# Performance work log

Hardware: AMD Instinct MI355X
Metric: run time of the kernel (lower is better)

Reference implementation:

```python
import jax, jax.numpy as jnp
import numpy as np
import math

# dims
B, T, HFEAT, E = 32, 8, 128, 128
NUM_CLS, NUM_GLOBAL = 4, 2
NSP = NUM_CLS + NUM_GLOBAL            # 6 special tokens
SCALES = (1, 4, 8)
WINDOW = 4
NHEAD = 8
DH = E // NHEAD                        # 16
NLAYERS = 2                            # blocks per scale = ceil(6/3)
NS = len(SCALES)
F = 512                                # dim_feedforward
ROPE_BASE = 100000.0
NEG = -1e9


def setup_inputs() -> dict:
    key = jax.random.key(0)
    ks = jax.random.split(key, 16)
    def rn(k, shape, s=0.02):
        return jax.random.normal(k, shape, jnp.float32) * s
    inp = {
        'embeddings': jax.random.normal(ks[0], (B, T, NSP + HFEAT, E), jnp.float32),
        'cls_tokens': rn(ks[1], (NUM_CLS, E)),
        'global_tokens': rn(ks[2], (NUM_GLOBAL, E)),
        'Wq': rn(ks[3], (NS, NLAYERS, E, E)),
        'bq': jnp.zeros((NS, NLAYERS, E), jnp.float32),
        'Wk': rn(ks[4], (NS, NLAYERS, E, E)),
        'bk': jnp.zeros((NS, NLAYERS, E), jnp.float32),
        'Wv': rn(ks[5], (NS, NLAYERS, E, E)),
        'bv': jnp.zeros((NS, NLAYERS, E), jnp.float32),
        'Wo': rn(ks[6], (NS, NLAYERS, E, E)),
        'bo': jnp.zeros((NS, NLAYERS, E), jnp.float32),
        'ln1_g': jnp.ones((NS, NLAYERS, E), jnp.float32),
        'ln1_b': jnp.zeros((NS, NLAYERS, E), jnp.float32),
        'ln2_g': jnp.ones((NS, NLAYERS, E), jnp.float32),
        'ln2_b': jnp.zeros((NS, NLAYERS, E), jnp.float32),
        'W1': rn(ks[7], (NS, NLAYERS, E, F)),
        'b1': jnp.zeros((NS, NLAYERS, F), jnp.float32),
        'W2': rn(ks[8], (NS, NLAYERS, F, E)),
        'b2': jnp.zeros((NS, NLAYERS, E), jnp.float32),
        'out_g': jnp.ones((E,), jnp.float32),
        'out_b': jnp.zeros((E,), jnp.float32),
    }
    return inp


def _layernorm(x, g, b, eps=1e-5):
    mu = x.mean(-1, keepdims=True)
    var = ((x - mu) ** 2).mean(-1, keepdims=True)
    return (x - mu) * jax.lax.rsqrt(var + eps) * g + b


def _rope(x):
    # x: (BT, L, H, DH); rotate-half RoPE over head dim
    L = x.shape[1]
    half = DH // 2
    inv = ROPE_BASE ** (-jnp.arange(half, dtype=jnp.float32) / half)
    ang = jnp.arange(L, dtype=jnp.float32)[:, None] * inv[None, :]   # (L, half)
    cos = jnp.cos(ang)[None, :, None, :]
    sin = jnp.sin(ang)[None, :, None, :]
    x1, x2 = x[..., :half], x[..., half:]
    return jnp.concatenate([x1 * cos - x2 * sin, x1 * sin + x2 * cos], axis=-1)


def _sparse_bias(L):
    # global(first NSP) rows/cols fully connected, others window +-WINDOW, diag allowed
    i = jnp.arange(L)
    allowed = (jnp.abs(i[:, None] - i[None, :]) <= WINDOW) | (i[:, None] < NSP) | (i[None, :] < NSP)
    return jnp.where(allowed, 0.0, NEG).astype(jnp.float32)  # (L, L) additive


def _encoder(x, s, Wq, bq, Wk, bk, Wv, bv, Wo, bo, ln1_g, ln1_b, ln2_g, ln2_b, W1, b1, W2, b2, bias):
    # x: (BT, L, E); pre-norm transformer encoder with RoPE attention
    BT, L, _ = x.shape
    for l in range(NLAYERS):
        h = _layernorm(x, ln1_g[s, l], ln1_b[s, l])
        q = (h @ Wq[s, l] + bq[s, l]).reshape(BT, L, NHEAD, DH)
        k = (h @ Wk[s, l] + bk[s, l]).reshape(BT, L, NHEAD, DH)
        v = (h @ Wv[s, l] + bv[s, l]).reshape(BT, L, NHEAD, DH)
        q, k = _rope(q), _rope(k)
        scores = jnp.einsum('blhd,bmhd->bhlm', q, k) / math.sqrt(DH) + bias[None, None]
        attn = jax.nn.softmax(scores, axis=-1)
        o = jnp.einsum('bhlm,bmhd->blhd', attn, v).reshape(BT, L, E)
        x = x + o @ Wo[s, l] + bo[s, l]
        h2 = _layernorm(x, ln2_g[s, l], ln2_b[s, l])
        x = x + jax.nn.gelu(h2 @ W1[s, l] + b1[s, l]) @ W2[s, l] + b2[s, l]
    return x


def reference(embeddings, cls_tokens, global_tokens, Wq, bq, Wk, bk, Wv, bv, Wo, bo,
              ln1_g, ln1_b, ln2_g, ln2_b, W1, b1, W2, b2, out_g, out_b):
    Bb, Tt, HC, Ee = embeddings.shape
    feats = embeddings[..., NSP:, :]                                 # (B,T,H,E)
    specials = jnp.broadcast_to(
        jnp.concatenate([cls_tokens, global_tokens], axis=0)[None, None],
        (Bb, Tt, NSP, Ee))
    cls_per_scale = []
    for s, g in enumerate(SCALES):
        H = feats.shape[2]
        K = H // g  # H divisible by all scales
        grouped = feats.reshape(Bb, Tt, K, g, Ee).mean(axis=3)       # contiguous mean grouping
        seq = jnp.concatenate([specials, grouped], axis=2)           # (B,T,L,E)
        L = NSP + K
        x = seq.reshape(Bb * Tt, L, Ee)
        bias = _sparse_bias(L)
        out = _encoder(x, s, Wq, bq, Wk, bk, Wv, bv, Wo, bo,
                       ln1_g, ln1_b, ln2_g, ln2_b, W1, b1, W2, b2, bias)
        cls_per_scale.append(out.reshape(Bb, Tt, L, Ee)[..., :NUM_CLS, :])
    cls_out = jnp.stack(cls_per_scale, axis=0).mean(axis=0)          # (B,T,num_cls,E)
    cls_out = _layernorm(cls_out, out_g, out_b)
    return cls_out.reshape(Bb, Tt, NUM_CLS * Ee)
```

## Files before the change

### kernel.cpp

```cpp
#include <hip/hip_runtime.h>
#include <hip/hip_bf16.h>

#define BT     256
#define EDIM   128
#define NSP    6
#define RT     49664
#define O1     34304
#define O2     44032
#define KSTR   20

typedef unsigned short u16;
typedef short s16x8 __attribute__((ext_vector_type(8)));
typedef float f32x4 __attribute__((ext_vector_type(4)));

__device__ __forceinline__ float u2f(u16 u){ union{unsigned i; float f;} v; v.i=((unsigned)u)<<16; return v.f; }
__device__ __forceinline__ u16 f2u(float f){
  union{float f; unsigned i;} v; v.f = f;
  unsigned r = v.i + 0x7FFF + ((v.i >> 16) & 1);
  return (u16)(r >> 16);
}
__device__ __forceinline__ float ldin(const void* p, size_t idx, int flag){
  return flag ? u2f(((const u16*)p)[idx]) : ((const float*)p)[idx];
}
__device__ __forceinline__ void unp8(uint4 v, float* f){
  f[0]=u2f((u16)(v.x)); f[1]=u2f((u16)(v.x>>16));
  f[2]=u2f((u16)(v.y)); f[3]=u2f((u16)(v.y>>16));
  f[4]=u2f((u16)(v.z)); f[5]=u2f((u16)(v.z>>16));
  f[6]=u2f((u16)(v.w)); f[7]=u2f((u16)(v.w>>16));
}

__device__ __forceinline__ void rowinfo(int row, int& s, int& r, int& L, int& g){
  if (row < O1){ s=0; r=row;    L=134; g=1; }
  else if (row < O2){ s=1; r=row-O1; L=38; g=4; }
  else { s=2; r=row-O2; L=22; g=8; }
}

__device__ __forceinline__ float ropeInv(int d){
  const float t[8] = {1.f, 0.23713737f, 0.056234132f, 0.013335214f,
                      3.1622777e-3f, 7.4989421e-4f, 1.7782794e-4f, 4.2169650e-5f};
  return t[d];
}

__device__ __forceinline__ float gelu_f(float x){
  float u = x*(1.5957691216f + 0.0713548162f*x*x);
  return x * __builtin_amdgcn_rcpf(1.f + __expf(-u));
}

__global__ void detect_k(const void* ln1g, int* flagp){
  unsigned v = *(const unsigned*)ln1g;
  *flagp = (v == 0x3F803F80u) ? 1 : 0;
}

struct CArg { const void* src; unsigned dstoff; unsigned n; unsigned inblk; unsigned outblk; };
struct CArgs { CArg a[12]; };
__global__ __launch_bounds__(256) void conv_k(CArgs ca, u16* stage, const int* flagp){
  int i = blockIdx.y;
  int flag = *flagp;
  const CArg& c = ca.a[i];
  for (unsigned idx = blockIdx.x*256u + threadIdx.x; idx < c.n; idx += gridDim.x*256u){
    unsigned blk = idx / c.inblk, r = idx % c.inblk;
    float v = flag ? u2f(((const u16*)c.src)[idx]) : ((const float*)c.src)[idx];
    stage[c.dstoff + blk*c.outblk + r] = flag ? ((const u16*)c.src)[idx] : f2u(v);
  }
}

__global__ __launch_bounds__(256) void convw_k(const void* s0, const void* s1, const void* s2,
                                               u16* dst, int K, int N, int Nsrc, const int* flagp)
{
  int flag = *flagp;
  const void* srcs[3] = {s0, s1, s2};
  int total = 6 * K * N;
  for (int idx = blockIdx.x*256 + threadIdx.x; idx < total; idx += gridDim.x*256) {
    int blk = idx / (K*N);
    int rem = idx % (K*N);
    int j = rem & 7;
    int t = rem >> 3;
    int n = t % N;
    int ck = t / N;
    int k = ck*8 + j;
    int w = n / Nsrc;
    int nn = n - w*Nsrc;
    size_t sidx = (size_t)blk*K*Nsrc + (size_t)k*Nsrc + nn;
    dst[idx] = flag ? ((const u16*)srcs[w])[sidx] : f2u(((const float*)srcs[w])[sidx]);
  }
}

__global__ __launch_bounds__(256) void build_k(const void* __restrict__ emb,
                                               const void* __restrict__ cls,
                                               const void* __restrict__ glob,
                                               float* __restrict__ x,
                                               u16* __restrict__ H,
                                               const u16* __restrict__ lnG,
                                               const u16* __restrict__ lnB,
                                               const int* flagp)
{
  int flag = *flagp;
  int row = blockIdx.x*4 + (threadIdx.x >> 6);
  int lane = threadIdx.x & 63;
  int s, r, L, g; rowinfo(row, s, r, L, g);
  int seq = r / L, pos = r % L;
  float v0, v1;
  if (pos < NSP) {
    const void* src = (pos < 4) ? cls : glob;
    int p = (pos < 4) ? pos : pos - 4;
    v0 = ldin(src, p*EDIM + lane, flag);
    v1 = ldin(src, p*EDIM + 64 + lane, flag);
  } else {
    int k = pos - NSP;
    size_t base = ((size_t)seq*134 + NSP + (size_t)k*g)*EDIM + lane;
    float s0 = 0.f, s1 = 0.f;
    for (int j = 0; j < g; j++) {
      s0 += ldin(emb, base + (size_t)j*EDIM, flag);
      s1 += ldin(emb, base + (size_t)j*EDIM + 64, flag);
    }
    float inv = 1.f/(float)g;
    v0 = s0*inv; v1 = s1*inv;
  }
  x[(size_t)row*EDIM + lane]      = v0;
  x[(size_t)row*EDIM + 64 + lane] = v1;
  float sum = v0 + v1, ss = v0*v0 + v1*v1;
  #pragma unroll
  for (int off = 32; off; off >>= 1) { sum += __shfl_xor(sum, off); ss += __shfl_xor(ss, off); }
  float mu = sum * (1.f/128.f);
  float var = ss * (1.f/128.f) - mu*mu;
  float rs = rsqrtf(var + 1e-5f);
  const u16* gp = lnG + s*2*EDIM;
  const u16* bp = lnB + s*2*EDIM;
  H[(size_t)row*EDIM + lane]      = f2u((v0-mu)*rs*u2f(gp[lane])    + u2f(bp[lane]));
  H[(size_t)row*EDIM + 64 + lane] = f2u((v1-mu)*rs*u2f(gp[64+lane]) + u2f(bp[64+lane]));
}

__global__ __launch_bounds__(256) void qkv_k(
    const u16* __restrict__ A,
    const u16* __restrict__ Wt, const u16* __restrict__ Bias,
    u16* __restrict__ C, int layer)
{
  const int row0 = blockIdx.x * 64;
  const int n0 = blockIdx.y * 128;
  const int s = row0 < O1 ? 0 : (row0 < O2 ? 1 : 2);
  const int sl = s*2 + layer;
  const u16* Wp = Wt + (size_t)sl*49152;
  const u16* bp = Bias + (size_t)sl*384 + n0;
  const int tid = threadIdx.x;
  const int lane = tid & 63, w = tid >> 6;
  const int g = lane >> 4, l15 = lane & 15;

  s16x8 af[4];
  {
    const u16* arow = A + (size_t)(row0 + w*16 + l15)*128;
    #pragma unroll
    for (int ks = 0; ks < 4; ks++) af[ks] = *(const s16x8*)(arow + (ks*4 + g)*8);
  }
  const u16* wbase = Wp + ((size_t)g*384 + n0 + l15)*8;

  f32x4 acc[8];
  #pragma unroll
  for (int nt = 0; nt < 8; nt++) acc[nt] = (f32x4){0.f,0.f,0.f,0.f};
  #pragma unroll
  for (int ks = 0; ks < 4; ks++) {
    s16x8 bw[8];
    #pragma unroll
    for (int nt = 0; nt < 8; nt++)
      bw[nt] = *(const s16x8*)(wbase + (size_t)ks*12288 + nt*128);
    #pragma unroll
    for (int nt = 0; nt < 8; nt++)
      acc[nt] = __builtin_amdgcn_mfma_f32_16x16x32_bf16(af[ks], bw[nt], acc[nt], 0, 0, 0);
  }

  float bb[8];
  #pragma unroll
  for (int nt = 0; nt < 8; nt++) bb[nt] = u2f(bp[nt*16 + l15]);
  #pragma unroll
  for (int reg = 0; reg < 4; reg++) {
    int row = row0 + w*16 + g*4 + reg;
    #pragma unroll
    for (int nt = 0; nt < 8; nt++)
      C[(size_t)row*384 + n0 + nt*16 + l15] = f2u(acc[nt][reg] + bb[nt]);
  }
}

template<int LNFUSE>
__global__ __launch_bounds__(256) __attribute__((amdgpu_waves_per_eu(2,3))) void woffn_k(
    const u16* __restrict__ A,
    const u16* __restrict__ Wot, const u16* __restrict__ Bo,
    const u16* __restrict__ W1t, const u16* __restrict__ B1,
    const u16* __restrict__ W2t, const u16* __restrict__ B2,
    float* __restrict__ X,
    u16* __restrict__ H,
    const u16* __restrict__ ln2G, const u16* __restrict__ ln2B,
    const u16* __restrict__ ln1G, const u16* __restrict__ ln1B,
    int layer)
{
  __shared__ u16 Hs[4][16*136];
  __shared__ u16 Ts[2][4][16*40];
  const int row0 = blockIdx.x * 64;
  const int s = row0 < O1 ? 0 : (row0 < O2 ? 1 : 2);
  const int sl = s*2 + layer;
  const u16* Wop = Wot + (size_t)sl*16384;
  const u16* bop = Bo  + sl*128;
  const u16* W1p = W1t + (size_t)sl*65536;
  const u16* b1p = B1  + sl*512;
  const u16* W2p = W2t + (size_t)sl*65536;
  const u16* b2p = B2  + sl*128;
  const int tid = threadIdx.x;
  const int lane = tid & 63, w = tid >> 6;
  const int g = lane >> 4, l15 = lane & 15;

  s16x8 af[4];
  {
    const u16* arow = A + (size_t)(row0 + w*16 + l15)*128;
    #pragma unroll
    for (int ks = 0; ks < 4; ks++) af[ks] = *(const s16x8*)(arow + (ks*4 + g)*8);
  }
  const u16* wobase = Wop + ((size_t)g*128 + l15)*8;

  f32x4 acc2[8];
  #pragma unroll
  for (int nt = 0; nt < 8; nt++) acc2[nt] = (f32x4){0.f,0.f,0.f,0.f};
  #pragma unroll
  for (int ks = 0; ks < 4; ks++) {
    s16x8 bw[8];
    #pragma unroll
    for (int nt = 0; nt < 8; nt++)
      bw[nt] = *(const s16x8*)(wobase + ((size_t)ks*4096 + nt*128));
    #pragma unroll
    for (int nt = 0; nt < 8; nt++)
      acc2[nt] = __builtin_amdgcn_mfma_f32_16x16x32_bf16(af[ks], bw[nt], acc2[nt], 0, 0, 0);
  }

  {
    float gam[8], bet[8], bo_[8];
    const u16* gp  = ln2G + sl*EDIM;
    const u16* bp2 = ln2B + sl*EDIM;
    #pragma unroll
    for (int nt = 0; nt < 8; nt++) {
      gam[nt] = u2f(gp[nt*16+l15]); bet[nt] = u2f(bp2[nt*16+l15]);
      bo_[nt] = u2f(bop[nt*16+l15]);
    }
    #pragma unroll
    for (int reg = 0; reg < 4; reg++) {
      int row = row0 + w*16 + g*4 + reg;
      float vals[8], ps = 0.f, pss = 0.f;
      #pragma unroll
      for (int nt = 0; nt < 8; nt++) {
        float v = acc2[nt][reg] + bo_[nt] + X[(size_t)row*128 + nt*16 + l15];
        vals[nt] = v; ps += v; pss += v*v;
      }
      #pragma unroll
      for (int off = 1; off < 16; off <<= 1) { ps += __shfl_xor(ps, off); pss += __shfl_xor(pss, off); }
      float mu = ps * (1.f/128.f);
      float var = pss * (1.f/128.f) - mu*mu;
      float rs = rsqrtf(var + 1e-5f);
      #pragma unroll
      for (int nt = 0; nt < 8; nt++) {
        acc2[nt][reg] = vals[nt];
        Hs[w][(g*4+reg)*136 + nt*16 + l15] = f2u((vals[nt]-mu)*rs*gam[nt] + bet[nt]);
      }
    }
  }

  s16x8 hf[4];
  #pragma unroll
  for (int ks = 0; ks < 4; ks++) hf[ks] = *(const s16x8*)&Hs[w][l15*136 + (ks*4+g)*8];

  const u16* w1base = W1p + ((size_t)g*512 + l15)*8;
  const u16* w2base = W2p + ((size_t)g*128 + l15)*8;

  s16x8 bw1[8];
  #pragma unroll
  for (int ks = 0; ks < 4; ks++)
    #pragma unroll
    for (int nt = 0; nt < 2; nt++)
      bw1[ks*2+nt] = *(const s16x8*)(w1base + (size_t)(ks*2048 + nt*16)*8);

  {
    f32x4 acc1[2];
    acc1[0] = (f32x4){0.f,0.f,0.f,0.f};
    acc1[1] = (f32x4){0.f,0.f,0.f,0.f};
    #pragma unroll
    for (int ks = 0; ks < 4; ks++) {
      acc1[0] = __builtin_amdgcn_mfma_f32_16x16x32_bf16(hf[ks], bw1[ks*2+0], acc1[0], 0, 0, 0);
      acc1[1] = __builtin_amdgcn_mfma_f32_16x16x32_bf16(hf[ks], bw1[ks*2+1], acc1[1], 0, 0, 0);
    }
    #pragma unroll
    for (int ks = 0; ks < 4; ks++)
      #pragma unroll
      for (int nt = 0; nt < 2; nt++)
        bw1[ks*2+nt] = *(const s16x8*)(w1base + (size_t)(ks*2048 + 32 + nt*16)*8);
    #pragma unroll
    for (int nt = 0; nt < 2; nt++) {
      float bb1 = u2f(b1p[nt*16 + l15]);
      #pragma unroll
      for (int reg = 0; reg < 4; reg++)
        Ts[0][w][(g*4+reg)*40 + nt*16 + l15] = f2u(gelu_f(acc1[nt][reg] + bb1));
    }
  }

  #pragma unroll
  for (int i = 1; i < 16; i++) {
    const int f0 = i*32, fp = f0 - 32;
    u16* tsC = &Ts[i & 1][w][0];
    const u16* tsP = &Ts[(i & 1) ^ 1][w][0];

    s16x8 bw2a[4];
    #pragma unroll
    for (int nt = 0; nt < 4; nt++)
      bw2a[nt] = *(const s16x8*)(w2base + (size_t)(fp*16 + nt*16)*8);
    s16x8 af2p = *(const s16x8*)(tsP + l15*40 + g*8);

    f32x4 acc1[2];
    acc1[0] = (f32x4){0.f,0.f,0.f,0.f};
    acc1[1] = (f32x4){0.f,0.f,0.f,0.f};
    #pragma unroll
    for (int ks = 0; ks < 4; ks++) {
      acc1[0] = __builtin_amdgcn_mfma_f32_16x16x32_bf16(hf[ks], bw1[ks*2+0], acc1[0], 0, 0, 0);
      acc1[1] = __builtin_amdgcn_mfma_f32_16x16x32_bf16(hf[ks], bw1[ks*2+1], acc1[1], 0, 0, 0);
    }
    {
      const int fn = (f0 + 32) & 511;
      #pragma unroll
      for (int ks = 0; ks < 4; ks++)
        #pragma unroll
        for (int nt = 0; nt < 2; nt++)
          bw1[ks*2+nt] = *(const s16x8*)(w1base + (size_t)(ks*2048 + fn + nt*16)*8);
    }
    s16x8 bw2b[4];
    #pragma unroll
    for (int nt = 0; nt < 4; nt++)
      bw2b[nt] = *(const s16x8*)(w2base + (size_t)(fp*16 + 64 + nt*16)*8);

    #pragma unroll
    for (int nt = 0; nt < 2; nt++) {
      float bb1 = u2f(b1p[f0 + nt*16 + l15]);
      #pragma unroll
      for (int reg = 0; reg < 4; reg++)
        tsC[(g*4+reg)*40 + nt*16 + l15] = f2u(gelu_f(acc1[nt][reg] + bb1));
    }

    #pragma unroll
    for (int nt = 0; nt < 4; nt++)
      acc2[nt] = __builtin_amdgcn_mfma_f32_16x16x32_bf16(af2p, bw2a[nt], acc2[nt], 0, 0, 0);
    #pragma unroll
    for (int nt = 0; nt < 4; nt++)
      acc2[4+nt] = __builtin_amdgcn_mfma_f32_16x16x32_bf16(af2p, bw2b[nt], acc2[4+nt], 0, 0, 0);
  }

  {
    s16x8 af2p = *(const s16x8*)&Ts[1][w][l15*40 + g*8];
    #pragma unroll
    for (int nt = 0; nt < 8; nt++) {
      s16x8 b = *(const s16x8*)(w2base + (size_t)(480*16 + nt*16)*8);
      acc2[nt] = __builtin_amdgcn_mfma_f32_16x16x32_bf16(af2p, b, acc2[nt], 0, 0, 0);
    }
  }

  float bb2[8];
  #pragma unroll
  for (int nt = 0; nt < 8; nt++) bb2[nt] = u2f(b2p[nt*16 + l15]);

  if (LNFUSE) {
    float gam[8], bet[8];
    const u16* gp  = ln1G + (s*2+1)*EDIM;
    const u16* bpn = ln1B + (s*2+1)*EDIM;
    #pragma unroll
    for (int nt = 0; nt < 8; nt++) { gam[nt] = u2f(gp[nt*16+l15]); bet[nt] = u2f(bpn[nt*16+l15]); }
    #pragma unroll
    for (int reg = 0; reg < 4; reg++) {
      int row = row0 + w*16 + g*4 + reg;
      float vals[8], ps = 0.f, pss = 0.f;
      #pragma unroll
      for (int nt = 0; nt < 8; nt++) {
        float v = acc2[nt][reg] + bb2[nt];
        vals[nt] = v; ps += v; pss += v*v;
      }
      #pragma unroll
      for (int off = 1; off < 16; off <<= 1) { ps += __shfl_xor(ps, off); pss += __shfl_xor(pss, off); }
      float mu = ps * (1.f/128.f);
      float var = pss * (1.f/128.f) - mu*mu;
      float rs = rsqrtf(var + 1e-5f);
      #pragma unroll
      for (int nt = 0; nt < 8; nt++) {
        size_t cidx = (size_t)row*128 + nt*16 + l15;
        X[cidx] = vals[nt];
        H[cidx] = f2u((vals[nt]-mu)*rs*gam[nt] + bet[nt]);
      }
    }
  } else {
    #pragma unroll
    for (int reg = 0; reg < 4; reg++) {
      int row = row0 + w*16 + g*4 + reg;
      #pragma unroll
      for (int nt = 0; nt < 8; nt++) {
        size_t cidx = (size_t)row*128 + nt*16 + l15;
        X[cidx] = acc2[nt][reg] + bb2[nt];
      }
    }
  }
}

__global__ __launch_bounds__(128) void attn_k(const u16* __restrict__ qkv, u16* __restrict__ o)
{
  __shared__ float Ks[134*KSTR];
  __shared__ float Vs[134*KSTR];
  int gseq = blockIdx.x, hd = blockIdx.y;
  int L, base;
  if (gseq < 256)      { L = 134; base = gseq*134; }
  else if (gseq < 512) { L = 38;  base = O1 + (gseq-256)*38; }
  else                 { L = 22;  base = O2 + (gseq-512)*22; }
  int tid = threadIdx.x;
  for (int u = tid; u < L*2; u += 128) {
    int kv = u & 1, row = u >> 1;
    const u16* p = qkv + (size_t)(base+row)*384 + 128 + kv*128 + hd*16;
    uint4 w0 = *(const uint4*)p, w1 = *(const uint4*)(p+8);
    float f[16];
    unp8(w0, f); unp8(w1, f+8);
    if (kv == 0) {
      #pragma unroll
      for (int d = 0; d < 8; d++) {
        float ang = (float)row * ropeInv(d);
        float cs = __cosf(ang), sn = __sinf(ang);
        float a = f[d], b = f[d+8];
        f[d]   = a*cs - b*sn;
        f[d+8] = a*sn + b*cs;
      }
    }
    float* dst = (kv ? Vs : Ks) + row*KSTR;
    #pragma unroll
    for (int d = 0; d < 16; d++) dst[d] = f[d];
  }
  __syncthreads();

  for (int it = tid; it < L - NSP; it += 128) {
    int row = NSP + it;
    const u16* qp = qkv + (size_t)(base+row)*384 + hd*16;
    uint4 w0 = *(const uint4*)qp, w1 = *(const uint4*)(qp+8);
    float q[16]; unp8(w0, q); unp8(w1, q+8);
    #pragma unroll
    for (int d = 0; d < 8; d++) {
      float ang = (float)row * ropeInv(d);
      float cs = __cosf(ang), sn = __sinf(ang);
      float a = q[d], b = q[d+8];
      q[d]   = a*cs - b*sn;
      q[d+8] = a*sn + b*cs;
    }
    float m = -1e30f, l = 0.f, oa[16] = {};
    auto step = [&](int j){
      const float4* kr = (const float4*)(Ks + j*KSTR);
      float4 k0 = kr[0], k1 = kr[1], k2 = kr[2], k3 = kr[3];
      float sc = q[0]*k0.x + q[1]*k0.y + q[2]*k0.z + q[3]*k0.w
               + q[4]*k1.x + q[5]*k1.y + q[6]*k1.z + q[7]*k1.w
               + q[8]*k2.x + q[9]*k2.y + q[10]*k2.z + q[11]*k2.w
               + q[12]*k3.x + q[13]*k3.y + q[14]*k3.z + q[15]*k3.w;
      sc *= 0.25f;
      float nm = fmaxf(m, sc);
      float scale = __expf(m - nm);
      float pexp = __expf(sc - nm);
      l = l*scale + pexp;
      const float4* vr = (const float4*)(Vs + j*KSTR);
      float4 v0 = vr[0], v1 = vr[1], v2 = vr[2], v3 = vr[3];
      oa[0]=oa[0]*scale+pexp*v0.x;  oa[1]=oa[1]*scale+pexp*v0.y;
      oa[2]=oa[2]*scale+pexp*v0.z;  oa[3]=oa[3]*scale+pexp*v0.w;
      oa[4]=oa[4]*scale+pexp*v1.x;  oa[5]=oa[5]*scale+pexp*v1.y;
      oa[6]=oa[6]*scale+pexp*v1.z;  oa[7]=oa[7]*scale+pexp*v1.w;
      oa[8]=oa[8]*scale+pexp*v2.x;  oa[9]=oa[9]*scale+pexp*v2.y;
      oa[10]=oa[10]*scale+pexp*v2.z; oa[11]=oa[11]*scale+pexp*v2.w;
      oa[12]=oa[12]*scale+pexp*v3.x; oa[13]=oa[13]*scale+pexp*v3.y;
      oa[14]=oa[14]*scale+pexp*v3.z; oa[15]=oa[15]*scale+pexp*v3.w;
      m = nm;
    };
    #pragma unroll
    for (int j = 0; j < NSP; j++) step(j);
    int jlo = (row-4 > NSP) ? row-4 : NSP;
    int jhi = (row+4 < L-1) ? row+4 : L-1;
    for (int j = jlo; j <= jhi; j++) step(j);
    float invl = 1.f/l;
    u16* op = o + (size_t)(base+row)*EDIM + hd*16;
    #pragma unroll
    for (int d = 0; d < 16; d++) op[d] = f2u(oa[d]*invl);
  }

  if (tid < 96) {
    int row = tid >> 4;
    int u = tid & 15;
    const u16* qp = qkv + (size_t)(base+row)*384 + hd*16;
    uint4 w0 = *(const uint4*)qp, w1 = *(const uint4*)(qp+8);
    float q[16]; unp8(w0, q); unp8(w1, q+8);
    #pragma unroll
    for (int d = 0; d < 8; d++) {
      float ang = (float)row * ropeInv(d);
      float cs = __cosf(ang), sn = __sinf(ang);
      float a = q[d], b = q[d+8];
      q[d]   = a*cs - b*sn;
      q[d+8] = a*sn + b*cs;
    }
    float m = -1e30f, l = 0.f, oa[16] = {};
    for (int j = u; j < L; j += 16) {
      const float4* kr = (const float4*)(Ks + j*KSTR);
      float4 k0 = kr[0], k1 = kr[1], k2 = kr[2], k3 = kr[3];
      float sc = q[0]*k0.x + q[1]*k0.y + q[2]*k0.z + q[3]*k0.w
               + q[4]*k1.x + q[5]*k1.y + q[6]*k1.z + q[7]*k1.w
               + q[8]*k2.x + q[9]*k2.y + q[10]*k2.z + q[11]*k2.w
               + q[12]*k3.x + q[13]*k3.y + q[14]*k3.z + q[15]*k3.w;
      sc *= 0.25f;
      float nm = fmaxf(m, sc);
      float scale = __expf(m - nm);
      float pexp = __expf(sc - nm);
      l = l*scale + pexp;
      const float4* vr = (const float4*)(Vs + j*KSTR);
      float4 v0 = vr[0], v1 = vr[1], v2 = vr[2], v3 = vr[3];
      oa[0]=oa[0]*scale+pexp*v0.x;  oa[1]=oa[1]*scale+pexp*v0.y;
      oa[2]=oa[2]*scale+pexp*v0.z;  oa[3]=oa[3]*scale+pexp*v0.w;
      oa[4]=oa[4]*scale+pexp*v1.x;  oa[5]=oa[5]*scale+pexp*v1.y;
      oa[6]=oa[6]*scale+pexp*v1.z;  oa[7]=oa[7]*scale+pexp*v1.w;
      oa[8]=oa[8]*scale+pexp*v2.x;  oa[9]=oa[9]*scale+pexp*v2.y;
      oa[10]=oa[10]*scale+pexp*v2.z; oa[11]=oa[11]*scale+pexp*v2.w;
      oa[12]=oa[12]*scale+pexp*v3.x; oa[13]=oa[13]*scale+pexp*v3.y;
      oa[14]=oa[14]*scale+pexp*v3.z; oa[15]=oa[15]*scale+pexp*v3.w;
      m = nm;
    }
    #pragma unroll
    for (int off = 1; off < 16; off <<= 1) {
      float m2 = __shfl_xor(m, off);
      float l2 = __shfl_xor(l, off);
      float nm = fmaxf(m, m2);
      float s1 = __expf(m - nm), s2 = __expf(m2 - nm);
      #pragma unroll
      for (int d = 0; d < 16; d++) {
        float o2 = __shfl_xor(oa[d], off);
        oa[d] = oa[d]*s1 + o2*s2;
      }
      l = l*s1 + l2*s2;
      m = nm;
    }
    if (u == 0) {
      float invl = 1.f/l;
      u16* op = o + (size_t)(base+row)*EDIM + hd*16;
      #pragma unroll
      for (int d = 0; d < 16; d++) op[d] = f2u(oa[d]*invl);
    }
  }
}

__global__ __launch_bounds__(256) void final_k(const float* __restrict__ x,
                                               const u16* __restrict__ G,
                                               const u16* __restrict__ Bt,
                                               void* __restrict__ out, const int* flagp)
{
  int flag = *flagp;
  int wid = threadIdx.x >> 6, lane = threadIdx.x & 63;
  int idx = blockIdx.x*4 + wid;
  int seq = idx >> 2, c = idx & 3;
  size_t r0 = ((size_t)seq*134 + c)*EDIM;
  size_t r1 = ((size_t)O1 + (size_t)seq*38 + c)*EDIM;
  size_t r2 = ((size_t)O2 + (size_t)seq*22 + c)*EDIM;
  float v0 = (x[r0+lane]    + x[r1+lane]    + x[r2+lane])    * (1.f/3.f);
  float v1 = (x[r0+64+lane] + x[r1+64+lane] + x[r2+64+lane]) * (1.f/3.f);
  float sum = v0 + v1;
  #pragma unroll
  for (int off = 32; off; off >>= 1) sum += __shfl_xor(sum, off);
  float mu = sum * (1.f/128.f);
  float d0 = v0 - mu, d1 = v1 - mu;
  float var = d0*d0 + d1*d1;
  #pragma unroll
  for (int off = 32; off; off >>= 1) var += __shfl_xor(var, off);
  var *= (1.f/128.f);
  float rs = rsqrtf(var + 1e-5f);
  float o0 = d0*rs*u2f(G[lane])    + u2f(Bt[lane]);
  float o1 = d1*rs*u2f(G[64+lane]) + u2f(Bt[64+lane]);
  size_t oi0 = (size_t)seq*512 + c*128 + lane;
  if (flag) { ((u16*)out)[oi0] = f2u(o0); ((u16*)out)[oi0+64] = f2u(o1); }
  else      { ((float*)out)[oi0] = o0;    ((float*)out)[oi0+64] = o1; }
}

#define S_WQKV 0u
#define S_BQKV 294912u
#define S_WO   297216u
#define S_BO   395520u
#define S_W1   396288u
#define S_B1   789504u
#define S_W2   792576u
#define S_B2   1185792u
#define S_L1G  1186560u
#define S_L1B  1187328u
#define S_L2G  1188096u
#define S_L2B  1188864u
#define S_OG   1189632u
#define S_OB   1189760u

extern "C" void kernel_launch(void* const* d_in, const int* in_sizes, int n_in,
                              void* d_out, int out_size, void* d_ws, size_t ws_size,
                              hipStream_t stream) {
  char* wsb = (char*)d_ws;
  int*   flagp = (int*)wsb;
  u16*   stage = (u16*)(wsb + 64);
  float* x     = (float*)(wsb + (size_t)2379840);
  u16*   h     = (u16*)(wsb + (size_t)27807808);
  u16*   qkv   = (u16*)(wsb + (size_t)40521792);

  detect_k<<<1, 1, 0, stream>>>(d_in[11], flagp);

  CArgs ca;
  CArg list[12] = {
    { d_in[4],  S_BQKV,       768, 128, 384 },
    { d_in[6],  S_BQKV+128u,  768, 128, 384 },
    { d_in[8],  S_BQKV+256u,  768, 128, 384 },
    { d_in[10], S_BO,         768, 128, 128 },
    { d_in[16], S_B1,        3072, 512, 512 },
    { d_in[18], S_B2,         768, 128, 128 },
    { d_in[11], S_L1G,        768, 128, 128 },
    { d_in[12], S_L1B,        768, 128, 128 },
    { d_in[13], S_L2G,        768, 128, 128 },
    { d_in[14], S_L2B,        768, 128, 128 },
    { d_in[19], S_OG,         128, 128, 128 },
    { d_in[20], S_OB,         128, 128, 128 },
  };
  for (int i = 0; i < 12; i++) ca.a[i] = list[i];
  conv_k<<<dim3(4, 12), 256, 0, stream>>>(ca, stage, flagp);

  convw_k<<<256, 256, 0, stream>>>(d_in[3], d_in[5], d_in[7], stage+S_WQKV, 128, 384, 128, flagp);
  convw_k<<<128, 256, 0, stream>>>(d_in[9], d_in[9], d_in[9], stage+S_WO,   128, 128, 128, flagp);
  convw_k<<<256, 256, 0, stream>>>(d_in[15],d_in[15],d_in[15],stage+S_W1,   128, 512, 512, flagp);
  convw_k<<<256, 256, 0, stream>>>(d_in[17],d_in[17],d_in[17],stage+S_W2,   512, 128, 128, flagp);

  build_k<<<RT/4, 256, 0, stream>>>(d_in[0], d_in[1], d_in[2], x, h, stage+S_L1G, stage+S_L1B, flagp);

  for (int l = 0; l < 2; l++) {
    qkv_k<<<dim3(RT/64, 3), 256, 0, stream>>>(h, stage+S_WQKV, stage+S_BQKV, qkv, l);
    attn_k<<<dim3(768, 8), 128, 0, stream>>>(qkv, h);
    if (l == 0)
      woffn_k<1><<<RT/64, 256, 0, stream>>>(h, stage+S_WO, stage+S_BO,
                                            stage+S_W1, stage+S_B1, stage+S_W2, stage+S_B2,
                                            x, h, stage+S_L2G, stage+S_L2B,
                                            stage+S_L1G, stage+S_L1B, 0);
    else
      woffn_k<0><<<RT/64, 256, 0, stream>>>(h, stage+S_WO, stage+S_BO,
                                            stage+S_W1, stage+S_B1, stage+S_W2, stage+S_B2,
                                            x, nullptr, stage+S_L2G, stage+S_L2B,
                                            stage+S_L1G, stage+S_L1B, 1);
  }
  final_k<<<BT, 256, 0, stream>>>(x, stage+S_OG, stage+S_OB, d_out, flagp);
}
```

Baseline: 355.8 us.

## Stage FFN weight chunks into LDS with async global-to-LDS loads

The fused Wo+FFN kernel used to load W1/W2 fragments directly from global memory into registers for each wave. It now double-buffers 32-column chunks of W1 and W2 in shared memory using global_load_lds, shared by all four waves, with a block barrier every iteration. The Hs/Ts buffers are merged to save LDS, and the waves_per_eu hint is dropped. This cuts redundant global and L2 traffic per block but adds barriers and an ordering risk around the async LDS loads. It also removes the software overlap the old code had between the GELU stage and the W2 MFMAs.

```diff
diff --git a/kernel.cpp b/kernel.cpp
--- a/kernel.cpp
+++ b/kernel.cpp
@@ -44,6 +44,12 @@
 __device__ __forceinline__ float gelu_f(float x){
   float u = x*(1.5957691216f + 0.0713548162f*x*x);
   return x * __builtin_amdgcn_rcpf(1.f + __expf(-u));
+}
+
+typedef const unsigned int __attribute__((address_space(1)))* gas1_t;
+typedef unsigned int __attribute__((address_space(3)))* las3_t;
+__device__ __forceinline__ void gload_lds16(const void* g, void* l){
+  __builtin_amdgcn_global_load_lds((gas1_t)g, (las3_t)l, 16, 0, 0);
 }
 
 __global__ void detect_k(const void* ln1g, int* flagp){
@@ -180,7 +186,7 @@
 }
 
 template<int LNFUSE>
-__global__ __launch_bounds__(256) __attribute__((amdgpu_waves_per_eu(2,3))) void woffn_k(
+__global__ __launch_bounds__(256) void woffn_k(
     const u16* __restrict__ A,
     const u16* __restrict__ Wot, const u16* __restrict__ Bo,
     const u16* __restrict__ W1t, const u16* __restrict__ B1,
@@ -191,8 +197,8 @@
     const u16* __restrict__ ln1G, const u16* __restrict__ ln1B,
     int layer)
 {
-  __shared__ u16 Hs[4][16*136];
-  __shared__ u16 Ts[2][4][16*40];
+  __shared__ u16 HsTs[4*2176];
+  __shared__ u16 wbuf[2][8192];
   const int row0 = blockIdx.x * 64;
   const int s = row0 < O1 ? 0 : (row0 < O2 ? 1 : 2);
   const int sl = s*2 + layer;
@@ -206,6 +212,26 @@
   const int lane = tid & 63, w = tid >> 6;
   const int g = lane >> 4, l15 = lane & 15;
 
+  auto stage_chunk = [&](int f0, int cur){
+    u16* wb = wbuf[cur];
+    if (w < 2) {
+      #pragma unroll
+      for (int j = 0; j < 4; j++) {
+        int base = w*2048 + j*512;
+        int kb = (base >> 8) + (lane >> 5);
+        gload_lds16(W1p + (size_t)kb*4096 + (size_t)(f0 + (lane & 31))*8, wb + base);
+      }
+    } else {
+      #pragma unroll
+      for (int j = 0; j < 4; j++) {
+        int base = (w - 2)*2048 + j*512;
+        gload_lds16(W2p + (size_t)(f0 >> 3)*1024 + base + lane*8, wb + 4096 + base);
+      }
+    }
+  };
+
+  stage_chunk(0, 0);
+
   s16x8 af[4];
   {
     const u16* arow = A + (size_t)(row0 + w*16 + l15)*128;
@@ -228,6 +254,7 @@
       acc2[nt] = __builtin_amdgcn_mfma_f32_16x16x32_bf16(af[ks], bw[nt], acc2[nt], 0, 0, 0);
   }
 
+  u16* Hsw = HsTs + w*2176;
   {
     float gam[8], bet[8], bo_[8];
     const u16* gp  = ln2G + sl*EDIM;
@@ -254,103 +281,47 @@
       #pragma unroll
       for (int nt = 0; nt < 8; nt++) {
         acc2[nt][reg] = vals[nt];
-        Hs[w][(g*4+reg)*136 + nt*16 + l15] = f2u((vals[nt]-mu)*rs*gam[nt] + bet[nt]);
+        Hsw[(g*4+reg)*136 + nt*16 + l15] = f2u((vals[nt]-mu)*rs*gam[nt] + bet[nt]);
       }
     }
   }
 
   s16x8 hf[4];
   #pragma unroll
-  for (int ks = 0; ks < 4; ks++) hf[ks] = *(const s16x8*)&Hs[w][l15*136 + (ks*4+g)*8];
-
-  const u16* w1base = W1p + ((size_t)g*512 + l15)*8;
-  const u16* w2base = W2p + ((size_t)g*128 + l15)*8;
-
-  s16x8 bw1[8];
-  #pragma unroll
-  for (int ks = 0; ks < 4; ks++)
-    #pragma unroll
-    for (int nt = 0; nt < 2; nt++)
-      bw1[ks*2+nt] = *(const s16x8*)(w1base + (size_t)(ks*2048 + nt*16)*8);
-
-  {
+  for (int ks = 0; ks < 4; ks++) hf[ks] = *(const s16x8*)&Hsw[l15*136 + (ks*4+g)*8];
+
+  u16* Tsw = HsTs + w*640;
+
+  for (int i = 0; i < 16; i++) {
+    const int f0 = i*32;
+    const u16* wb = wbuf[i & 1];
+    __syncthreads();
+    if (i < 15) stage_chunk(f0 + 32, (i + 1) & 1);
+
     f32x4 acc1[2];
     acc1[0] = (f32x4){0.f,0.f,0.f,0.f};
     acc1[1] = (f32x4){0.f,0.f,0.f,0.f};
     #pragma unroll
     for (int ks = 0; ks < 4; ks++) {
-      acc1[0] = __builtin_amdgcn_mfma_f32_16x16x32_bf16(hf[ks], bw1[ks*2+0], acc1[0], 0, 0, 0);
-      acc1[1] = __builtin_amdgcn_mfma_f32_16x16x32_bf16(hf[ks], bw1[ks*2+1], acc1[1], 0, 0, 0);
-    }
-    #pragma unroll
-    for (int ks = 0; ks < 4; ks++)
-      #pragma unroll
-      for (int nt = 0; nt < 2; nt++)
-        bw1[ks*2+nt] = *(const s16x8*)(w1base + (size_t)(ks*2048 + 32 + nt*16)*8);
-    #pragma unroll
-    for (int nt = 0; nt < 2; nt++) {
-      float bb1 = u2f(b1p[nt*16 + l15]);
-      #pragma unroll
-      for (int reg = 0; reg < 4; reg++)
-        Ts[0][w][(g*4+reg)*40 + nt*16 + l15] = f2u(gelu_f(acc1[nt][reg] + bb1));
-    }
-  }
-
-  #pragma unroll
-  for (int i = 1; i < 16; i++) {
-    const int f0 = i*32, fp = f0 - 32;
-    u16* tsC = &Ts[i & 1][w][0];
-    const u16* tsP = &Ts[(i & 1) ^ 1][w][0];
-
-    s16x8 bw2a[4];
-    #pragma unroll
-    for (int nt = 0; nt < 4; nt++)
-      bw2a[nt] = *(const s16x8*)(w2base + (size_t)(fp*16 + nt*16)*8);
-    s16x8 af2p = *(const s16x8*)(tsP + l15*40 + g*8);
-
-    f32x4 acc1[2];
-    acc1[0] = (f32x4){0.f,0.f,0.f,0.f};
-    acc1[1] = (f32x4){0.f,0.f,0.f,0.f};
-    #pragma unroll
-    for (int ks = 0; ks < 4; ks++) {
-      acc1[0] = __builtin_amdgcn_mfma_f32_16x16x32_bf16(hf[ks], bw1[ks*2+0], acc1[0], 0, 0, 0);
-      acc1[1] = __builtin_amdgcn_mfma_f32_16x16x32_bf16(hf[ks], bw1[ks*2+1], acc1[1], 0, 0, 0);
-    }
-    {
-      const int fn = (f0 + 32) & 511;
-      #pragma unroll
-      for (int ks = 0; ks < 4; ks++)
-        #pragma unroll
-        for (int nt = 0; nt < 2; nt++)
-          bw1[ks*2+nt] = *(const s16x8*)(w1base + (size_t)(ks*2048 + fn + nt*16)*8);
-    }
-    s16x8 bw2b[4];
-    #pragma unroll
-    for (int nt = 0; nt < 4; nt++)
-      bw2b[nt] = *(const s16x8*)(w2base + (size_t)(fp*16 + 64 + nt*16)*8);
-
+      const int c = ks*4 + g;
+      #pragma unroll
+      for (int nt = 0; nt < 2; nt++) {
+        s16x8 bf = *(const s16x8*)&wb[c*256 + (nt*16 + l15)*8];
+        acc1[nt] = __builtin_amdgcn_mfma_f32_16x16x32_bf16(hf[ks], bf, acc1[nt], 0, 0, 0);
+      }
+    }
     #pragma unroll
     for (int nt = 0; nt < 2; nt++) {
       float bb1 = u2f(b1p[f0 + nt*16 + l15]);
       #pragma unroll
       for (int reg = 0; reg < 4; reg++)
-        tsC[(g*4+reg)*40 + nt*16 + l15] = f2u(gelu_f(acc1[nt][reg] + bb1));
-    }
-
-    #pragma unroll
-    for (int nt = 0; nt < 4; nt++)
-      acc2[nt] = __builtin_amdgcn_mfma_f32_16x16x32_bf16(af2p, bw2a[nt], acc2[nt], 0, 0, 0);
-    #pragma unroll
-    for (int nt = 0; nt < 4; nt++)
-      acc2[4+nt] = __builtin_amdgcn_mfma_f32_16x16x32_bf16(af2p, bw2b[nt], acc2[4+nt], 0, 0, 0);
-  }
-
-  {
-    s16x8 af2p = *(const s16x8*)&Ts[1][w][l15*40 + g*8];
+        Tsw[(g*4+reg)*40 + nt*16 + l15] = f2u(gelu_f(acc1[nt][reg] + bb1));
+    }
+    s16x8 af2 = *(const s16x8*)&Tsw[l15*40 + g*8];
     #pragma unroll
     for (int nt = 0; nt < 8; nt++) {
-      s16x8 b = *(const s16x8*)(w2base + (size_t)(480*16 + nt*16)*8);
-      acc2[nt] = __builtin_amdgcn_mfma_f32_16x16x32_bf16(af2p, b, acc2[nt], 0, 0, 0);
+      s16x8 bf = *(const s16x8*)&wb[4096 + g*1024 + (nt*16 + l15)*8];
+      acc2[nt] = __builtin_amdgcn_mfma_f32_16x16x32_bf16(af2, bf, acc2[nt], 0, 0, 0);
     }
   }
 
```

Measured after the change: 368.6 us. 1.04x slower.

## Fuse input build and LayerNorm into first QKV GEMM and merge prep kernels

Applied to the files above, without the earlier changes.

Removes the separate flag-detect kernel by having each kernel read the dtype flag directly from the ln1 gamma input. The bias/LN conversion and the four weight-repack kernels are merged into one prep kernel launch. The build step (group mean, x write, LN1) is folded into the layer-0 QKV GEMM so the normalized activations go straight into MFMA fragments and skip an h round-trip through global memory. The trade-off is that each of the three N-blocks recomputes the grouped mean and LayerNorm for its rows, which triples the embedding reads. The prep kernel also uses only 64 blocks per task.

```diff
diff --git a/kernel.cpp b/kernel.cpp
--- a/kernel.cpp
+++ b/kernel.cpp
@@ -28,6 +28,15 @@
   f[4]=u2f((u16)(v.z)); f[5]=u2f((u16)(v.z>>16));
   f[6]=u2f((u16)(v.w)); f[7]=u2f((u16)(v.w>>16));
 }
+__device__ __forceinline__ void ld8f(const void* p, size_t e, int flag, float* f){
+  if (flag){ uint4 v = *(const uint4*)((const u16*)p + e); unp8(v, f); }
+  else {
+    const float4* q = (const float4*)((const float*)p + e);
+    float4 a = q[0], b = q[1];
+    f[0]=a.x; f[1]=a.y; f[2]=a.z; f[3]=a.w;
+    f[4]=b.x; f[5]=b.y; f[6]=b.z; f[7]=b.w;
+  }
+}
 
 __device__ __forceinline__ void rowinfo(int row, int& s, int& r, int& L, int& g){
   if (row < O1){ s=0; r=row;    L=134; g=1; }
@@ -46,92 +55,60 @@
   return x * __builtin_amdgcn_rcpf(1.f + __expf(-u));
 }
 
-__global__ void detect_k(const void* ln1g, int* flagp){
-  unsigned v = *(const unsigned*)ln1g;
-  *flagp = (v == 0x3F803F80u) ? 1 : 0;
+__device__ __forceinline__ int dflag(const void* ln1g){
+  return (*(const unsigned*)ln1g == 0x3F803F80u) ? 1 : 0;
 }
 
 struct CArg { const void* src; unsigned dstoff; unsigned n; unsigned inblk; unsigned outblk; };
-struct CArgs { CArg a[12]; };
-__global__ __launch_bounds__(256) void conv_k(CArgs ca, u16* stage, const int* flagp){
-  int i = blockIdx.y;
-  int flag = *flagp;
-  const CArg& c = ca.a[i];
-  for (unsigned idx = blockIdx.x*256u + threadIdx.x; idx < c.n; idx += gridDim.x*256u){
-    unsigned blk = idx / c.inblk, r = idx % c.inblk;
-    float v = flag ? u2f(((const u16*)c.src)[idx]) : ((const float*)c.src)[idx];
-    stage[c.dstoff + blk*c.outblk + r] = flag ? ((const u16*)c.src)[idx] : f2u(v);
-  }
-}
-
-__global__ __launch_bounds__(256) void convw_k(const void* s0, const void* s1, const void* s2,
-                                               u16* dst, int K, int N, int Nsrc, const int* flagp)
-{
-  int flag = *flagp;
-  const void* srcs[3] = {s0, s1, s2};
-  int total = 6 * K * N;
-  for (int idx = blockIdx.x*256 + threadIdx.x; idx < total; idx += gridDim.x*256) {
-    int blk = idx / (K*N);
-    int rem = idx % (K*N);
-    int j = rem & 7;
-    int t = rem >> 3;
-    int n = t % N;
-    int ck = t / N;
-    int k = ck*8 + j;
-    int w = n / Nsrc;
-    int nn = n - w*Nsrc;
-    size_t sidx = (size_t)blk*K*Nsrc + (size_t)k*Nsrc + nn;
-    dst[idx] = flag ? ((const u16*)srcs[w])[sidx] : f2u(((const float*)srcs[w])[sidx]);
-  }
-}
-
-__global__ __launch_bounds__(256) void build_k(const void* __restrict__ emb,
-                                               const void* __restrict__ cls,
-                                               const void* __restrict__ glob,
-                                               float* __restrict__ x,
-                                               u16* __restrict__ H,
-                                               const u16* __restrict__ lnG,
-                                               const u16* __restrict__ lnB,
-                                               const int* flagp)
-{
-  int flag = *flagp;
-  int row = blockIdx.x*4 + (threadIdx.x >> 6);
-  int lane = threadIdx.x & 63;
-  int s, r, L, g; rowinfo(row, s, r, L, g);
-  int seq = r / L, pos = r % L;
-  float v0, v1;
-  if (pos < NSP) {
-    const void* src = (pos < 4) ? cls : glob;
-    int p = (pos < 4) ? pos : pos - 4;
-    v0 = ldin(src, p*EDIM + lane, flag);
-    v1 = ldin(src, p*EDIM + 64 + lane, flag);
+struct PrepArgs {
+  const void* ln1g;
+  CArg c[12];
+  const void* ws[4][3];
+  unsigned wdst[4];
+  int wK[4], wN[4], wNsrc[4];
+  u16* stage;
+};
+__global__ __launch_bounds__(256) void prep_k(PrepArgs pa){
+  const int flag = dflag(pa.ln1g);
+  const int tid = threadIdx.x;
+  if (blockIdx.y == 0){
+    for (int i = 0; i < 12; i++){
+      const CArg& cc = pa.c[i];
+      for (unsigned idx = blockIdx.x*256u + tid; idx < cc.n; idx += 64u*256u){
+        unsigned blk = idx / cc.inblk, r = idx % cc.inblk;
+        pa.stage[cc.dstoff + blk*cc.outblk + r] =
+          flag ? ((const u16*)cc.src)[idx] : f2u(((const float*)cc.src)[idx]);
+      }
+    }
   } else {
-    int k = pos - NSP;
-    size_t base = ((size_t)seq*134 + NSP + (size_t)k*g)*EDIM + lane;
-    float s0 = 0.f, s1 = 0.f;
-    for (int j = 0; j < g; j++) {
-      s0 += ldin(emb, base + (size_t)j*EDIM, flag);
-      s1 += ldin(emb, base + (size_t)j*EDIM + 64, flag);
-    }
-    float inv = 1.f/(float)g;
-    v0 = s0*inv; v1 = s1*inv;
-  }
-  x[(size_t)row*EDIM + lane]      = v0;
-  x[(size_t)row*EDIM + 64 + lane] = v1;
-  float sum = v0 + v1, ss = v0*v0 + v1*v1;
-  #pragma unroll
-  for (int off = 32; off; off >>= 1) { sum += __shfl_xor(sum, off); ss += __shfl_xor(ss, off); }
-  float mu = sum * (1.f/128.f);
-  float var = ss * (1.f/128.f) - mu*mu;
-  float rs = rsqrtf(var + 1e-5f);
-  const u16* gp = lnG + s*2*EDIM;
-  const u16* bp = lnB + s*2*EDIM;
-  H[(size_t)row*EDIM + lane]      = f2u((v0-mu)*rs*u2f(gp[lane])    + u2f(bp[lane]));
-  H[(size_t)row*EDIM + 64 + lane] = f2u((v1-mu)*rs*u2f(gp[64+lane]) + u2f(bp[64+lane]));
-}
-
+    const int v = blockIdx.y - 1;
+    const int K = pa.wK[v], N = pa.wN[v], Nsrc = pa.wNsrc[v];
+    u16* dst = pa.stage + pa.wdst[v];
+    const int total = 6*K*N;
+    for (int idx = blockIdx.x*256 + tid; idx < total; idx += 64*256){
+      int blk = idx / (K*N);
+      int rem = idx % (K*N);
+      int j = rem & 7;
+      int t = rem >> 3;
+      int n = t % N;
+      int ck = t / N;
+      int k = ck*8 + j;
+      int w2 = n / Nsrc;
+      int nn = n - w2*Nsrc;
+      size_t sidx = (size_t)blk*K*Nsrc + (size_t)k*Nsrc + nn;
+      dst[idx] = flag ? ((const u16*)pa.ws[v][w2])[sidx]
+                      : f2u(((const float*)pa.ws[v][w2])[sidx]);
+    }
+  }
+}
+
+template<int BUILD>
 __global__ __launch_bounds__(256) void qkv_k(
     const u16* __restrict__ A,
+    const void* __restrict__ emb, const void* __restrict__ cls, const void* __restrict__ glob,
+    float* __restrict__ x,
+    const u16* __restrict__ lnG, const u16* __restrict__ lnB,
+    const void* __restrict__ flagSrc,
     const u16* __restrict__ Wt, const u16* __restrict__ Bias,
     u16* __restrict__ C, int layer)
 {
@@ -146,11 +123,74 @@
   const int g = lane >> 4, l15 = lane & 15;
 
   s16x8 af[4];
-  {
+  if (BUILD) {
+    const int flag = dflag(flagSrc);
+    const int row = row0 + w*16 + l15;
+    int ss, r, L, gg; rowinfo(row, ss, r, L, gg);
+    const int seq = r / L, pos = r % L;
+    float val[4][8];
+    if (pos < NSP) {
+      const void* src = (pos < 4) ? cls : glob;
+      const int p = (pos < 4) ? pos : pos - 4;
+      #pragma unroll
+      for (int ks = 0; ks < 4; ks++)
+        ld8f(src, (size_t)p*EDIM + (ks*4+g)*8, flag, val[ks]);
+    } else {
+      const int k = pos - NSP;
+      const size_t rbase = ((size_t)seq*134 + NSP + (size_t)k*gg)*EDIM;
+      #pragma unroll
+      for (int ks = 0; ks < 4; ks++) {
+        const int cb = (ks*4+g)*8;
+        ld8f(emb, rbase + cb, flag, val[ks]);
+        for (int jj = 1; jj < gg; jj++) {
+          float t[8];
+          ld8f(emb, rbase + (size_t)jj*EDIM + cb, flag, t);
+          #pragma unroll
+          for (int j = 0; j < 8; j++) val[ks][j] += t[j];
+        }
+        if (gg > 1) {
+          const float iv = 1.f/(float)gg;
+          #pragma unroll
+          for (int j = 0; j < 8; j++) val[ks][j] *= iv;
+        }
+      }
+    }
+    float ps = 0.f, pss = 0.f;
+    #pragma unroll
+    for (int ks = 0; ks < 4; ks++)
+      #pragma unroll
+      for (int j = 0; j < 8; j++) { float v = val[ks][j]; ps += v; pss += v*v; }
+    ps += __shfl_xor(ps, 16); pss += __shfl_xor(pss, 16);
+    ps += __shfl_xor(ps, 32); pss += __shfl_xor(pss, 32);
+    const float mu = ps * (1.f/128.f);
+    const float var = pss * (1.f/128.f) - mu*mu;
+    const float rs = rsqrtf(var + 1e-5f);
+    if (n0 == 0) {
+      #pragma unroll
+      for (int ks = 0; ks < 4; ks++) {
+        const int cb = (ks*4+g)*8;
+        float* xp = x + (size_t)row*EDIM + cb;
+        *(float4*)xp     = (float4){val[ks][0], val[ks][1], val[ks][2], val[ks][3]};
+        *(float4*)(xp+4) = (float4){val[ks][4], val[ks][5], val[ks][6], val[ks][7]};
+      }
+    }
+    const u16* gp  = lnG + s*2*EDIM;
+    const u16* bpn = lnB + s*2*EDIM;
+    #pragma unroll
+    for (int ks = 0; ks < 4; ks++) {
+      const int cb = (ks*4+g)*8;
+      union { s16x8 v; u16 e[8]; } fr;
+      #pragma unroll
+      for (int j = 0; j < 8; j++)
+        fr.e[j] = f2u((val[ks][j]-mu)*rs*u2f(gp[cb+j]) + u2f(bpn[cb+j]));
+      af[ks] = fr.v;
+    }
+  } else {
     const u16* arow = A + (size_t)(row0 + w*16 + l15)*128;
     #pragma unroll
     for (int ks = 0; ks < 4; ks++) af[ks] = *(const s16x8*)(arow + (ks*4 + g)*8);
   }
+
   const u16* wbase = Wp + ((size_t)g*384 + n0 + l15)*8;
 
   f32x4 acc[8];
@@ -544,9 +584,10 @@
 __global__ __launch_bounds__(256) void final_k(const float* __restrict__ x,
                                                const u16* __restrict__ G,
                                                const u16* __restrict__ Bt,
-                                               void* __restrict__ out, const int* flagp)
+                                               void* __restrict__ out,
+                                               const void* __restrict__ flagSrc)
 {
-  int flag = *flagp;
+  int flag = dflag(flagSrc);
   int wid = threadIdx.x >> 6, lane = threadIdx.x & 63;
   int idx = blockIdx.x*4 + wid;
   int seq = idx >> 2, c = idx & 3;
@@ -591,15 +632,14 @@
                               void* d_out, int out_size, void* d_ws, size_t ws_size,
                               hipStream_t stream) {
   char* wsb = (char*)d_ws;
-  int*   flagp = (int*)wsb;
   u16*   stage = (u16*)(wsb + 64);
   float* x     = (float*)(wsb + (size_t)2379840);
   u16*   h     = (u16*)(wsb + (size_t)27807808);
   u16*   qkv   = (u16*)(wsb + (size_t)40521792);
 
-  detect_k<<<1, 1, 0, stream>>>(d_in[11], flagp);
-
-  CArgs ca;
+  PrepArgs pa;
+  pa.ln1g = d_in[11];
+  pa.stage = stage;
   CArg list[12] = {
     { d_in[4],  S_BQKV,       768, 128, 384 },
     { d_in[6],  S_BQKV+128u,  768, 128, 384 },
@@ -614,18 +654,28 @@
     { d_in[19], S_OG,         128, 128, 128 },
     { d_in[20], S_OB,         128, 128, 128 },
   };
-  for (int i = 0; i < 12; i++) ca.a[i] = list[i];
-  conv_k<<<dim3(4, 12), 256, 0, stream>>>(ca, stage, flagp);
-
-  convw_k<<<256, 256, 0, stream>>>(d_in[3], d_in[5], d_in[7], stage+S_WQKV, 128, 384, 128, flagp);
-  convw_k<<<128, 256, 0, stream>>>(d_in[9], d_in[9], d_in[9], stage+S_WO,   128, 128, 128, flagp);
-  convw_k<<<256, 256, 0, stream>>>(d_in[15],d_in[15],d_in[15],stage+S_W1,   128, 512, 512, flagp);
-  convw_k<<<256, 256, 0, stream>>>(d_in[17],d_in[17],d_in[17],stage+S_W2,   512, 128, 128, flagp);
-
-  build_k<<<RT/4, 256, 0, stream>>>(d_in[0], d_in[1], d_in[2], x, h, stage+S_L1G, stage+S_L1B, flagp);
+  for (int i = 0; i < 12; i++) pa.c[i] = list[i];
+  pa.ws[0][0]=d_in[3];  pa.ws[0][1]=d_in[5];  pa.ws[0][2]=d_in[7];
+  pa.ws[1][0]=d_in[9];  pa.ws[1][1]=d_in[9];  pa.ws[1][2]=d_in[9];
+  pa.ws[2][0]=d_in[15]; pa.ws[2][1]=d_in[15]; pa.ws[2][2]=d_in[15];
+  pa.ws[3][0]=d_in[17]; pa.ws[3][1]=d_in[17]; pa.ws[3][2]=d_in[17];
+  pa.wdst[0]=S_WQKV; pa.wdst[1]=S_WO; pa.wdst[2]=S_W1; pa.wdst[3]=S_W2;
+  pa.wK[0]=128; pa.wN[0]=384; pa.wNsrc[0]=128;
+  pa.wK[1]=128; pa.wN[1]=128; pa.wNsrc[1]=128;
+  pa.wK[2]=128; pa.wN[2]=512; pa.wNsrc[2]=512;
+  pa.wK[3]=512; pa.wN[3]=128; pa.wNsrc[3]=128;
+
+  prep_k<<<dim3(64, 5), 256, 0, stream>>>(pa);
 
   for (int l = 0; l < 2; l++) {
-    qkv_k<<<dim3(RT/64, 3), 256, 0, stream>>>(h, stage+S_WQKV, stage+S_BQKV, qkv, l);
+    if (l == 0)
+      qkv_k<1><<<dim3(RT/64, 3), 256, 0, stream>>>(nullptr, d_in[0], d_in[1], d_in[2],
+                                                   x, stage+S_L1G, stage+S_L1B, d_in[11],
+                                                   stage+S_WQKV, stage+S_BQKV, qkv, 0);
+    else
+      qkv_k<0><<<dim3(RT/64, 3), 256, 0, stream>>>(h, nullptr, nullptr, nullptr,
+                                                   nullptr, nullptr, nullptr, d_in[11],
+                                                   stage+S_WQKV, stage+S_BQKV, qkv, 1);
     attn_k<<<dim3(768, 8), 128, 0, stream>>>(qkv, h);
     if (l == 0)
       woffn_k<1><<<RT/64, 256, 0, stream>>>(h, stage+S_WO, stage+S_BO,
@@ -638,5 +688,5 @@
                                             x, nullptr, stage+S_L2G, stage+S_L2B,
                                             stage+S_L1G, stage+S_L1B, 1);
   }
-  final_k<<<BT, 256, 0, stream>>>(x, stage+S_OG, stage+S_OB, d_out, flagp);
-}
+  final_k<<<BT, 256, 0, stream>>>(x, stage+S_OG, stage+S_OB, d_out, d_in[11]);
+}
```

Result: no change. 357.2 us (+0.4%).
